# Kernel optimization log

Hardware: AMD Instinct MI355X
Metric: run time of the kernel (lower is better)

The kernel has to match this reference:

```python
import jax, jax.numpy as jnp
import numpy as np

R = 131072   # rays
S = 128      # existing samples per ray (existing_bins has S+1 edges)
N_NEW = 64   # new importance samples per ray
HIST_PAD = 1e-5   # NeuSSampler builds PDFSampler(histogram_padding=1e-5)
EPS = 1e-5


def setup_inputs() -> dict:
    key = jax.random.key(0)
    k1, k2, k3, k4 = jax.random.split(key, 4)
    weights = jax.random.uniform(k1, (R, S, 1), dtype=jnp.float32)
    # existing spacing bins must be sorted in [0,1] along the sample axis
    existing_bins = jnp.sort(jax.random.uniform(k2, (R, S + 1), dtype=jnp.float32), axis=-1)
    nears = 0.05 + 0.5 * jax.random.uniform(k3, (R, 1), dtype=jnp.float32)
    fars = nears + 1.0 + 3.0 * jax.random.uniform(k4, (R, 1), dtype=jnp.float32)
    return {"weights": weights, "existing_bins": existing_bins,
            "nears": nears, "fars": fars, "num_samples": N_NEW}


def reference(weights, existing_bins, nears, fars, num_samples):
    # PDFSampler.generate_ray_samples core (eval mode, include_original=False)
    num_bins = num_samples + 1
    w = weights[..., 0] + HIST_PAD                      # [R, S]
    w_sum = jnp.sum(w, axis=-1, keepdims=True)          # [R, 1]
    padding = jax.nn.relu(EPS - w_sum)
    w = w + padding / w.shape[-1]
    w_sum = w_sum + padding
    pdf = w / w_sum                                     # [R, S]
    cdf = jnp.minimum(jnp.ones_like(pdf), jnp.cumsum(pdf, axis=-1))
    cdf = jnp.concatenate([jnp.zeros_like(cdf[..., :1]), cdf], axis=-1)  # [R, S+1]

    # deterministic mid-bin query points (non-stratified branch)
    u = jnp.linspace(0.0, 1.0 - 1.0 / num_bins, num_bins, dtype=cdf.dtype)
    u = u + 1.0 / (2 * num_bins)
    u = jnp.broadcast_to(u, (*cdf.shape[:-1], num_bins))  # [R, num_bins]

    # inverse-CDF: per-ray binary search + gather + linear interp
    inds = jax.vmap(lambda c, q: jnp.searchsorted(c, q, side='right'))(cdf, u)
    last = existing_bins.shape[-1] - 1
    below = jnp.clip(inds - 1, 0, last)
    above = jnp.clip(inds, 0, last)
    cdf_g0 = jnp.take_along_axis(cdf, below, axis=-1)
    bins_g0 = jnp.take_along_axis(existing_bins, below, axis=-1)
    cdf_g1 = jnp.take_along_axis(cdf, above, axis=-1)
    bins_g1 = jnp.take_along_axis(existing_bins, above, axis=-1)
    t = jnp.clip(jnp.nan_to_num((u - cdf_g0) / (cdf_g1 - cdf_g0), nan=0.0,
                                posinf=0.0, neginf=0.0), 0.0, 1.0)
    bins = bins_g0 + t * (bins_g1 - bins_g0)            # [R, num_bins]
    bins = jax.lax.stop_gradient(bins)                  # torch: bins.detach()

    # spacing_to_euclidean_fn for UniformSampler: x*s_far + (1-x)*s_near
    euclidean_bins = bins * fars + (1.0 - bins) * nears  # [R, num_bins]
    return euclidean_bins
```

## Files before the change

### kernel.cpp

```cpp
#include <hip/hip_runtime.h>


#define DPP_FADD(x, ctrl, rmask)                                             \
    ((x) + __int_as_float(__builtin_amdgcn_update_dpp(                       \
               0, __float_as_int(x), (ctrl), (rmask), 0xf, true)))

__global__ __launch_bounds__(256) void neus_sampler_kernel(
    const float* __restrict__ weights,
    const float* __restrict__ bins_g,
    const float* __restrict__ nears,
    const float* __restrict__ fars,
    float* __restrict__ out,
    int R)
{
    constexpr int S  = 128;
    constexpr int NB = 65;
    constexpr float HPAD = 1e-5f;

    __shared__ float4 pay[4][NB];

    const int lane = threadIdx.x & 63;
    const int wv   = threadIdx.x >> 6;
    const int ray  = blockIdx.x * 4 + wv;
    if (ray >= R) return;
    const int uray = __builtin_amdgcn_readfirstlane(ray);

    const float2 wpair =
        reinterpret_cast<const float2*>(weights + (size_t)uray * S)[lane];
    const float* brow = bins_g + (size_t)uray * (S + 1);
    const float2 bpair = reinterpret_cast<const float2*>(brow)[lane];
    const float b_last = brow[S];

    const float w1 = wpair.y + HPAD;
    float ps = (wpair.x + HPAD) + w1;

    ps = DPP_FADD(ps, 0x111, 0xf);
    ps = DPP_FADD(ps, 0x112, 0xf);
    ps = DPP_FADD(ps, 0x114, 0xf);
    ps = DPP_FADD(ps, 0x118, 0xf);
    ps = DPP_FADD(ps, 0x142, 0xa);
    ps = DPP_FADD(ps, 0x143, 0xc);

    const float total =
        __int_as_float(__builtin_amdgcn_readlane(__float_as_int(ps), 63));
    const float padding = fmaxf(1e-5f - total, 0.0f);
    const float padc    = padding * (1.0f / S);
    const float inv     = __builtin_amdgcn_rcpf(total + padding);

    const float c_hi  = fminf(1.0f, fmaf((float)(2 * lane + 2), padc, ps) * inv);
    const float c_mid = fminf(1.0f, fmaf((float)(2 * lane + 1), padc, ps - w1) * inv);
    float c_lo = __shfl_up(c_hi, 1, 64);
    if (lane == 0) c_lo = 0.0f;
    float b2 = __shfl_down(bpair.x, 1, 64);
    if (lane == 63) b2 = b_last;

    const float nearv = nears[uray];
    const float farv  = fars[uray];
    const float fmn   = farv - nearv;

    auto jf = [](float c) -> int {
        int j = (int)ceilf(fmaf(65.0f, c, -0.5f));
        return j < 0 ? 0 : (j > NB ? NB : j);
    };

    const int j0 = jf(c_lo);
    const int j2 = (lane == 63) ? NB : jf(c_hi);
    int j1 = jf(c_mid);
    j1 = j1 < j0 ? j0 : (j1 > j2 ? j2 : j1);

    float4* const wp = &pay[wv][0];

    if (j1 > j0) {
        const float r = __builtin_amdgcn_rcpf(c_mid - c_lo);
        const float4 v = make_float4(c_lo, r,
                                     fmaf(bpair.x, fmn, nearv),
                                     (bpair.y - bpair.x) * fmn);
        for (int j = j0; j < j1; ++j) wp[j] = v;
    }
    if (j2 > j1) {
        const float r = __builtin_amdgcn_rcpf(c_hi - c_mid);
        const float4 v = make_float4(c_mid, r,
                                     fmaf(bpair.y, fmn, nearv),
                                     (b2 - bpair.y) * fmn);
        for (int j = j1; j < j2; ++j) wp[j] = v;
    }

    asm volatile("s_waitcnt lgkmcnt(0)" ::: "memory");

    float* const orow = out + (size_t)uray * NB;
    {
        const float4 p  = wp[lane];
        const float  u  = (float)(2 * lane + 1) * (1.0f / 130.0f);
        const float  t  = (u - p.x) * p.y;
        const float  tc = fminf(fmaxf(t, 0.0f), 1.0f);
        orow[lane] = fmaf(tc, p.w, p.z);
    }
    if (lane == 0) {
        const float4 p  = wp[64];
        const float  t  = (129.0f / 130.0f - p.x) * p.y;
        const float  tc = fminf(fmaxf(t, 0.0f), 1.0f);
        orow[64] = fmaf(tc, p.w, p.z);
    }
}

extern "C" void kernel_launch(void* const* d_in, const int* in_sizes, int n_in,
                              void* d_out, int out_size, void* d_ws, size_t ws_size,
                              hipStream_t stream) {
    const float* weights = (const float*)d_in[0];
    const float* ebins   = (const float*)d_in[1];
    const float* nears   = (const float*)d_in[2];
    const float* fars    = (const float*)d_in[3];
    float* out = (float*)d_out;
    const int R = in_sizes[0] / 128;
    const int blocks = (R + 3) / 4;
    hipLaunchKernelGGL(neus_sampler_kernel, dim3(blocks), dim3(256), 0, stream,
                       weights, ebins, nears, fars, out, R);
}
```

Measured before the change: 163.3 us.

## Replace per-lane fill loops with atomicMax scatter plus wave prefix-max

Instead of each lane writing its segment payload into every query slot it covers (variable-length loops causing divergence), each lane writes its two segment payloads once, records its segment index at the query slot via LDS atomicMax, and a DPP prefix-max scan recovers, for every query, the last segment starting at or before it. The reciprocal of the segment width is computed at read time rather than write time. This removes divergent loop trip counts, but it adds LDS atomics, zeroing of the index table and extra LDS storage. Correctness relies on the intra-wave LDS ordering between the zeroing, the atomics and the reads, with no barrier.

After: 162.5 us. No clear change (-0.5%).

```diff
diff --git a/kernel.cpp b/kernel.cpp
--- a/kernel.cpp
+++ b/kernel.cpp
@@ -4,6 +4,14 @@
 #define DPP_FADD(x, ctrl, rmask)                                             \
     ((x) + __int_as_float(__builtin_amdgcn_update_dpp(                       \
                0, __float_as_int(x), (ctrl), (rmask), 0xf, true)))
+
+#define DPP_UMAX(x, ctrl, rmask)                                             \
+    (umax_((x), (unsigned)__builtin_amdgcn_update_dpp(                       \
+               0, (int)(x), (ctrl), (rmask), 0xf, true)))
+
+__device__ __forceinline__ unsigned umax_(unsigned a, unsigned b) {
+    return a > b ? a : b;
+}
 
 __global__ __launch_bounds__(256) void neus_sampler_kernel(
     const float* __restrict__ weights,
@@ -17,13 +25,17 @@
     constexpr int NB = 65;
     constexpr float HPAD = 1e-5f;
 
-    __shared__ float4 pay[4][NB];
+    __shared__ float4   pay[4][S];
+    __shared__ unsigned best[4][66];
 
     const int lane = threadIdx.x & 63;
     const int wv   = threadIdx.x >> 6;
     const int ray  = blockIdx.x * 4 + wv;
     if (ray >= R) return;
     const int uray = __builtin_amdgcn_readfirstlane(ray);
+
+    if (lane < 33)
+        *reinterpret_cast<unsigned long long*>(&best[wv][2 * lane]) = 0ull;
 
     const float2 wpair =
         reinterpret_cast<const float2*>(weights + (size_t)uray * S)[lane];
@@ -58,46 +70,41 @@
     const float farv  = fars[uray];
     const float fmn   = farv - nearv;
 
+    pay[wv][2 * lane] = make_float4(
+        c_lo, c_mid - c_lo, fmaf(bpair.x, fmn, nearv), (bpair.y - bpair.x) * fmn);
+    pay[wv][2 * lane + 1] = make_float4(
+        c_mid, c_hi - c_mid, fmaf(bpair.y, fmn, nearv), (b2 - bpair.y) * fmn);
+
     auto jf = [](float c) -> int {
         int j = (int)ceilf(fmaf(65.0f, c, -0.5f));
         return j < 0 ? 0 : (j > NB ? NB : j);
     };
 
-    const int j0 = jf(c_lo);
-    const int j2 = (lane == 63) ? NB : jf(c_hi);
-    int j1 = jf(c_mid);
-    j1 = j1 < j0 ? j0 : (j1 > j2 ? j2 : j1);
-
-    float4* const wp = &pay[wv][0];
-
-    if (j1 > j0) {
-        const float r = __builtin_amdgcn_rcpf(c_mid - c_lo);
-        const float4 v = make_float4(c_lo, r,
-                                     fmaf(bpair.x, fmn, nearv),
-                                     (bpair.y - bpair.x) * fmn);
-        for (int j = j0; j < j1; ++j) wp[j] = v;
-    }
-    if (j2 > j1) {
-        const float r = __builtin_amdgcn_rcpf(c_hi - c_mid);
-        const float4 v = make_float4(c_mid, r,
-                                     fmaf(bpair.y, fmn, nearv),
-                                     (b2 - bpair.y) * fmn);
-        for (int j = j1; j < j2; ++j) wp[j] = v;
-    }
+    atomicMax(&best[wv][jf(c_lo)],  (unsigned)(2 * lane));
+    atomicMax(&best[wv][jf(c_mid)], (unsigned)(2 * lane + 1));
 
     asm volatile("s_waitcnt lgkmcnt(0)" ::: "memory");
 
+    unsigned m = best[wv][lane];
+    m = DPP_UMAX(m, 0x111, 0xf);
+    m = DPP_UMAX(m, 0x112, 0xf);
+    m = DPP_UMAX(m, 0x114, 0xf);
+    m = DPP_UMAX(m, 0x118, 0xf);
+    m = DPP_UMAX(m, 0x142, 0xa);
+    m = DPP_UMAX(m, 0x143, 0xc);
+
     float* const orow = out + (size_t)uray * NB;
     {
-        const float4 p  = wp[lane];
+        const float4 p  = pay[wv][m];
         const float  u  = (float)(2 * lane + 1) * (1.0f / 130.0f);
-        const float  t  = (u - p.x) * p.y;
+        const float  t  = (u - p.x) * __builtin_amdgcn_rcpf(p.y);
         const float  tc = fminf(fmaxf(t, 0.0f), 1.0f);
         orow[lane] = fmaf(tc, p.w, p.z);
     }
-    if (lane == 0) {
-        const float4 p  = wp[64];
-        const float  t  = (129.0f / 130.0f - p.x) * p.y;
+    if (lane == 63) {
+        const unsigned m64 = umax_(m, best[wv][64]);
+        const float4 p  = pay[wv][m64];
+        const float  t  = (129.0f / 130.0f - p.x) * __builtin_amdgcn_rcpf(p.y);
         const float  tc = fminf(fmaxf(t, 0.0f), 1.0f);
         orow[64] = fmaf(tc, p.w, p.z);
     }
```
